# Kernel tuning notes

Hardware: AMD Instinct MI355X
Metric: run time of the kernel (lower is better)

The kernel has to match this reference:

```python
import jax, jax.numpy as jnp
import numpy as np

V_WORD, V_ENT, V_REL = 50000, 200000, 1000
B, S, CTX, T = 64, 128, 256, 10
E, D, H, C = 300, 100, 256, 3  # input_dim, triples_embedding_dim, hidden, classes
IN = E + 2 * D  # LSTM input size in graph_attention mode


def setup_inputs() -> dict:
    key = jax.random.key(0)
    ks = jax.random.split(key, 16)
    inputs = jax.random.randint(ks[0], (B, S), 0, V_WORD)
    context = jax.random.randint(ks[1], (B, CTX), 0, V_WORD)
    triples = jax.random.randint(ks[2], (B, S, T, 3), 0, V_REL)
    lengths = jax.random.randint(ks[3], (B,), 1, S + 1)  # valid lengths >= 1
    # id2_ids_batch: -1 sentinel means "no triple"; mix of -1 and valid
    id2_ids_batch = jax.random.randint(ks[4], (B, S, T), 0, 2) * 2 - 1
    embedding = jax.random.normal(ks[5], (V_WORD, E), jnp.float32) * 0.02
    embeddings_entity = jax.random.normal(ks[6], (V_ENT, D), jnp.float32) * 0.02
    embeddings_relation = jax.random.normal(ks[7], (V_REL, D), jnp.float32) * 0.02
    W_ent = jax.random.normal(ks[8], (D, 2 * D), jnp.float32) * 0.05  # entity_transformed (no bias)
    W_ih = jax.random.normal(ks[9], (4 * H, IN), jnp.float32) * 0.05
    W_hh = jax.random.normal(ks[10], (4 * H, H), jnp.float32) * 0.05
    b_lstm = jnp.zeros((4 * H,), jnp.float32)
    attn_w = jax.random.normal(ks[11], (1, H), jnp.float32) * 0.05
    attn_b = jnp.zeros((1,), jnp.float32)
    out_w = jax.random.normal(ks[12], (C, H), jnp.float32) * 0.05
    out_b = jnp.zeros((C,), jnp.float32)
    return dict(inputs=inputs, context=context, triples=triples, lengths=lengths,
                id2_ids_batch=id2_ids_batch, embedding=embedding,
                embeddings_entity=embeddings_entity, embeddings_relation=embeddings_relation,
                W_ent=W_ent, W_ih=W_ih, W_hh=W_hh, b_lstm=b_lstm,
                attn_w=attn_w, attn_b=attn_b, out_w=out_w, out_b=out_b)


def _lstm(x, W_ih, W_hh, b):
    """Single-layer unidirectional LSTM, PyTorch gate order (i,f,g,o). x: [B,S,I] -> [B,S,H]."""
    Hh = W_hh.shape[1]
    xg = jnp.einsum('bsi,gi->bsg', x, W_ih) + b  # precompute input projections [B,S,4H]
    def step(carry, xg_t):
        h, c = carry
        g = xg_t + h @ W_hh.T
        i, f, gg, o = jnp.split(g, 4, axis=-1)
        c = jax.nn.sigmoid(f) * c + jax.nn.sigmoid(i) * jnp.tanh(gg)
        h = jax.nn.sigmoid(o) * jnp.tanh(c)
        return (h, c), h
    h0 = jnp.zeros((x.shape[0], Hh), x.dtype)
    _, hs = jax.lax.scan(step, (h0, h0), jnp.swapaxes(xg, 0, 1))
    return jnp.swapaxes(hs, 0, 1)


def reference(inputs, context, triples, lengths, id2_ids_batch, embedding,
              embeddings_entity, embeddings_relation, W_ent, W_ih, W_hh, b_lstm,
              attn_w, attn_b, out_w, out_b):
    x = embedding[inputs]  # [B,S,E]
    # graph_attention branch, vectorized over (batch, token, triple)
    eh = embeddings_entity[triples[..., 0]]   # [B,S,T,D]
    et = embeddings_entity[triples[..., 1]]   # [B,S,T,D]
    er = embeddings_relation[triples[..., 2]] # [B,S,T,D]
    ht = jnp.concatenate([eh, et], axis=-1)   # [B,S,T,2D]
    tr = jnp.tanh(jnp.einsum('bstk,dk->bstd', ht, W_ent))  # entity_transformed + tanh
    e = jnp.sum(tr * er, axis=-1)             # [B,S,T]
    alpha = jax.nn.softmax(e, axis=-1)        # softmax over triples
    graph = jnp.einsum('bst,bstk->bsk', alpha, ht)  # [B,S,2D]
    valid = jnp.any(id2_ids_batch != -1, axis=-1)   # [B,S]; all -1 -> zeros (cc branch)
    graph = jnp.where(valid[..., None], graph, 0.0)
    t_in = jnp.concatenate([x, graph], axis=-1)     # [B,S,E+2D]
    out = _lstm(t_in, W_ih, W_hh, b_lstm)           # [B,S,H]
    # 'att' attention pooling, masked by lengths (pack/pad equivalent)
    mask = jnp.arange(S)[None, :] < lengths[:, None]
    scores = (jnp.einsum('bsh,oh->bso', out, attn_w) + attn_b)[..., 0]  # [B,S]
    a = jax.nn.softmax(jnp.where(mask, scores, -1e9), axis=-1)
    attended = jnp.einsum('bs,bsh->bh', a, out)     # [B,H]
    logits = attended @ out_w.T + out_b             # [B,C]
    return logits
```

## Files before the change

### kernel.cpp

```cpp
#include <hip/hip_runtime.h>
#include <cstdint>
#include <cstddef>

typedef unsigned int  uint_t;
typedef unsigned short ushort_t;

constexpr int B_  = 64;
constexpr int S_  = 128;
constexpr int D_  = 100;
constexpr int E_  = 300;
constexpr int H_  = 256;
constexpr int KIN = 512;
constexpr int NG  = 1024;
constexpr int M_  = B_ * S_;

constexpr int RW = 48;
constexpr int LW = 16;

constexpr size_t OFF_WT   = 0;
constexpr size_t OFF_FLAG = 40000;
constexpr size_t OFF_WIH  = 40960;
constexpr size_t OFF_WHH  = OFF_WIH + (size_t)NG * KIN * 2;
constexpr size_t OFF_TIN  = OFF_WHH + (size_t)128 * NG * 4;
constexpr size_t OFF_XG   = OFF_TIN + (size_t)M_ * KIN * 2;
constexpr size_t OFF_HOUT = OFF_XG + (size_t)M_ * NG * 4;

__device__ __forceinline__ float b2f(ushort_t u) {
  union { uint_t u; float f; } v; v.u = ((uint_t)u) << 16; return v.f;
}
__device__ __forceinline__ float blo(uint_t u) {
  union { uint_t u; float f; } v; v.u = u << 16; return v.f;
}
__device__ __forceinline__ float bhi(uint_t u) {
  union { uint_t u; float f; } v; v.u = u & 0xffff0000u; return v.f;
}
__device__ __forceinline__ ushort_t f2b(float f) {
  union { float f; uint_t u; } v; v.f = f;
  uint_t r = (v.u + 0x7fffu + ((v.u >> 16) & 1u)) >> 16;
  return (ushort_t)r;
}
__device__ __forceinline__ ushort_t f16bits(float f) {
  _Float16 h = (_Float16)f;
  union { _Float16 h; ushort_t u; } v; v.h = h; return v.u;
}
__device__ __forceinline__ uint_t pk16(float a, float b) {
  return (uint_t)f16bits(a) | ((uint_t)f16bits(b) << 16);
}
__device__ __forceinline__ float fast_tanh(float x) {
  float e = __expf(2.f * x);
  return 1.f - 2.f / (e + 1.f);
}
__device__ __forceinline__ float sigm(float x) {
  return 1.f / (1.f + __expf(-x));
}
__device__ __forceinline__ float ldv(const void* p, size_t i, int f32) {
  return f32 ? ((const float*)p)[i] : b2f(((const ushort_t*)p)[i]);
}

#if defined(__has_builtin)
#if __has_builtin(__builtin_amdgcn_fdot2)
#define HAVE_FDOT2 1
#endif
#endif

typedef _Float16 half2v __attribute__((ext_vector_type(2)));

__device__ __forceinline__ float dot2(uint_t w, uint_t h, float acc) {
#ifdef HAVE_FDOT2
  union { uint_t u; half2v v; } a, b; a.u = w; b.u = h;
  return __builtin_amdgcn_fdot2(a.v, b.v, acc, false);
#else
  union { uint_t u; _Float16 h[2]; } a, b; a.u = w; b.u = h;
  acc += (float)a.h[0] * (float)b.h[0];
  acc += (float)a.h[1] * (float)b.h[1];
  return acc;
#endif
}

__global__ __launch_bounds__(64) void k_detect(const uint_t* __restrict__ emb_w,
                                               char* __restrict__ ws)
{
  int tid = threadIdx.x;
  int hits = 0;
  for (int i = 0; i < 8; ++i) {
    uint_t w = emb_w[i * 64 + tid];
    uint_t e = (w >> 7) & 0xffu;
    hits += (e >= 140) ? 1 : 0;
  }
  for (int off = 32; off > 0; off >>= 1) hits += __shfl_down(hits, off);
  if (tid == 0) *(int*)(ws + OFF_FLAG) = (hits >= 32) ? 1 : 0;
}

__global__ __launch_bounds__(256) void k0_prep(
    const void* __restrict__ W_ent, const void* __restrict__ W_ih,
    const void* __restrict__ W_hh, char* __restrict__ ws)
{
  const int f32 = *(const int*)(ws + OFF_FLAG);
  int id = blockIdx.x * 256 + threadIdx.x;
  uint_t*   Wt = (uint_t*)(ws + OFF_WT);
  ushort_t* Wp = (ushort_t*)(ws + OFF_WIH);
  uint_t*   WT = (uint_t*)(ws + OFF_WHH);
  if (id < 10000) {
    int kp = id / 100, d = id % 100;
    float a = ldv(W_ent, (size_t)d * 200 + 2 * kp,     f32);
    float b = ldv(W_ent, (size_t)d * 200 + 2 * kp + 1, f32);
    Wt[id] = pk16(a, b);
  } else if (id >= 20000 && id < 20000 + NG * KIN) {
    int i = id - 20000;
    int n = i >> 9, k = i & 511;
    Wp[i] = (k < 500) ? f2b(ldv(W_ih, (size_t)n * 500 + k, f32)) : (ushort_t)0;
  } else if (id >= 20000 + NG * KIN && id < 20000 + NG * KIN + 128 * NG) {
    int i = id - 20000 - NG * KIN;
    int kk = i >> 10, j = i & 1023;
    ushort_t lo = f16bits(ldv(W_hh, (size_t)j * 256 + 2 * kk,     f32));
    ushort_t hi = f16bits(ldv(W_hh, (size_t)j * 256 + 2 * kk + 1, f32));
    WT[kk * 1024 + j] = (uint_t)lo | ((uint_t)hi << 16);
  }
}

__global__ __launch_bounds__(512) void k1_graph(
    const int* __restrict__ inputs, const int* __restrict__ triples,
    const int* __restrict__ id2, const void* __restrict__ emb,
    const void* __restrict__ ent, const void* __restrict__ rel,
    char* __restrict__ ws)
{
  __shared__ __align__(16) uint_t Wl2[10000];
  __shared__ uint_t htp[4][10][100];
  __shared__ float er_l[4][10][100];
  __shared__ float e_l[4][10];
  __shared__ float alpha_l[4][10];
  __shared__ int   trip_l[4][30];
  __shared__ int   vflag[4];

  const int tid = threadIdx.x;
  const int j   = tid >> 7;
  const int lt  = tid & 127;
  const int m   = blockIdx.x * 4 + j;
  const int f32 = *(const int*)(ws + OFF_FLAG);
  ushort_t* tin = (ushort_t*)(ws + OFF_TIN);

  if (lt < 30) trip_l[j][lt] = triples[(size_t)m * 30 + lt];
  if (lt == 0) vflag[j] = 0;
  if (lt < 10) e_l[j][lt] = 0.f;
  __syncthreads();
  if (lt < 10 && id2[(size_t)m * 10 + lt] != -1) atomicOr(&vflag[j], 1);

  {
    const uint4* src = (const uint4*)(ws + OFF_WT);
    uint4* dst = (uint4*)Wl2;
    for (int i = tid; i < 2500; i += 512) dst[i] = src[i];
  }
  for (int i = lt; i < 1000; i += 128) {
    int t = i / 100, kp = i % 100;
    int row = trip_l[j][t * 3 + (kp < 50 ? 0 : 1)];
    int off = (kp < 50) ? 2 * kp : 2 * (kp - 50);
    float x0, x1;
    if (f32) {
      float2 v = *(const float2*)((const float*)ent + (size_t)row * 100 + off);
      x0 = v.x; x1 = v.y;
    } else {
      uint_t u = *(const uint_t*)((const ushort_t*)ent + (size_t)row * 100 + off);
      x0 = blo(u); x1 = bhi(u);
    }
    htp[j][t][kp] = pk16(x0, x1);
  }
  for (int i = lt; i < 1000; i += 128) {
    int t = i / 100, d = i % 100;
    er_l[j][t][d] = ldv(rel, (size_t)trip_l[j][t * 3 + 2] * 100 + d, f32);
  }
  {
    int w = inputs[m];
    for (int c = lt; c < 300; c += 128)
      tin[(size_t)m * KIN + c] = f2b(ldv(emb, (size_t)w * E_ + c, f32));
    if (lt < 12) tin[(size_t)m * KIN + 500 + lt] = 0;
  }
  __syncthreads();

  if (lt < 125) {
    int t2 = lt / 25, d4 = lt % 25;
    int t0 = 2 * t2, t1 = t0 + 1;
    const uint_t* h0p = htp[j][t0];
    const uint_t* h1p = htp[j][t1];
    float a00 = 0, a01 = 0, a02 = 0, a03 = 0;
    float a10 = 0, a11 = 0, a12 = 0, a13 = 0;
    for (int kp = 0; kp < 100; ++kp) {
      uint4 wv = *(const uint4*)&Wl2[kp * 100 + 4 * d4];
      uint_t hp0 = h0p[kp], hp1 = h1p[kp];
      a00 = dot2(wv.x, hp0, a00); a01 = dot2(wv.y, hp0, a01);
      a02 = dot2(wv.z, hp0, a02); a03 = dot2(wv.w, hp0, a03);
      a10 = dot2(wv.x, hp1, a10); a11 = dot2(wv.y, hp1, a11);
      a12 = dot2(wv.z, hp1, a12); a13 = dot2(wv.w, hp1, a13);
    }
    int d = 4 * d4;
    float s0 = fast_tanh(a00) * er_l[j][t0][d]     + fast_tanh(a01) * er_l[j][t0][d + 1]
             + fast_tanh(a02) * er_l[j][t0][d + 2] + fast_tanh(a03) * er_l[j][t0][d + 3];
    float s1 = fast_tanh(a10) * er_l[j][t1][d]     + fast_tanh(a11) * er_l[j][t1][d + 1]
             + fast_tanh(a12) * er_l[j][t1][d + 2] + fast_tanh(a13) * er_l[j][t1][d + 3];
    atomicAdd(&e_l[j][t0], s0);
    atomicAdd(&e_l[j][t1], s1);
  }
  __syncthreads();
  if (lt == 0) {
    float mx = e_l[j][0];
    for (int t = 1; t < 10; ++t) mx = fmaxf(mx, e_l[j][t]);
    float s = 0.f;
    for (int t = 0; t < 10; ++t) { float v = __expf(e_l[j][t] - mx); alpha_l[j][t] = v; s += v; }
    float inv = 1.f / s;
    for (int t = 0; t < 10; ++t) alpha_l[j][t] *= inv;
  }
  __syncthreads();
  for (int kp = lt; kp < 100; kp += 128) {
    float g0 = 0.f, g1 = 0.f;
#pragma unroll
    for (int t = 0; t < 10; ++t) {
      union { uint_t u; _Float16 h[2]; } v; v.u = htp[j][t][kp];
      g0 += alpha_l[j][t] * (float)v.h[0];
      g1 += alpha_l[j][t] * (float)v.h[1];
    }
    if (!vflag[j]) { g0 = 0.f; g1 = 0.f; }
    tin[(size_t)m * KIN + 300 + 2 * kp]     = f2b(g0);
    tin[(size_t)m * KIN + 300 + 2 * kp + 1] = f2b(g1);
  }
}

typedef __attribute__((ext_vector_type(8))) short short8;
typedef __attribute__((ext_vector_type(4))) float f32x4;

__global__ __launch_bounds__(256) void k2_xg(
    const void* __restrict__ bl, char* __restrict__ ws)
{
  __shared__ __align__(16) ushort_t As[128 * 32];
  __shared__ __align__(16) ushort_t Bs[128 * 32];
  const ushort_t* A  = (const ushort_t*)(ws + OFF_TIN);
  const ushort_t* Bw = (const ushort_t*)(ws + OFF_WIH);
  float* xg = (float*)(ws + OFF_XG);
  const int f32 = *(const int*)(ws + OFF_FLAG);

  const int tid = threadIdx.x;
  const int m0 = blockIdx.x * 128;
  const int n0 = blockIdx.y * 128;
  const int lane = tid & 63, wv = tid >> 6;
  const int wm = wv & 1, wn = wv >> 1;
  const int g = lane >> 4, r = lane & 15;

  f32x4 acc[4][4] = {};

  for (int ks = 0; ks < 16; ++ks) {
    const int k0 = ks * 32;
    {
      int c0 = tid, c1 = tid + 256;
      uint4 a0 = *(const uint4*)(A  + (size_t)(m0 + (c0 >> 2)) * KIN + k0 + ((c0 & 3) << 3));
      uint4 a1 = *(const uint4*)(A  + (size_t)(m0 + (c1 >> 2)) * KIN + k0 + ((c1 & 3) << 3));
      uint4 b0 = *(const uint4*)(Bw + (size_t)(n0 + (c0 >> 2)) * KIN + k0 + ((c0 & 3) << 3));
      uint4 b1 = *(const uint4*)(Bw + (size_t)(n0 + (c1 >> 2)) * KIN + k0 + ((c1 & 3) << 3));
      ((uint4*)As)[c0] = a0; ((uint4*)As)[c1] = a1;
      ((uint4*)Bs)[c0] = b0; ((uint4*)Bs)[c1] = b1;
    }
    __syncthreads();
    short8 av[4], bv[4];
#pragma unroll
    for (int i = 0; i < 4; ++i)
      av[i] = *(const short8*)&As[(wm * 64 + i * 16 + r) * 32 + g * 8];
#pragma unroll
    for (int j = 0; j < 4; ++j)
      bv[j] = *(const short8*)&Bs[(wn * 64 + j * 16 + r) * 32 + g * 8];
#pragma unroll
    for (int i = 0; i < 4; ++i)
#pragma unroll
      for (int j = 0; j < 4; ++j)
        acc[i][j] = __builtin_amdgcn_mfma_f32_16x16x32_bf16(av[i], bv[j], acc[i][j], 0, 0, 0);
    __syncthreads();
  }
#pragma unroll
  for (int j = 0; j < 4; ++j) {
    int n = n0 + wn * 64 + j * 16 + r;
    float bias = ldv(bl, n, f32);
#pragma unroll
    for (int i = 0; i < 4; ++i) {
      int mrow = m0 + wm * 64 + i * 16 + g * 4;
#pragma unroll
      for (int rr = 0; rr < 4; ++rr)
        xg[(size_t)(mrow + rr) * NG + n] = acc[i][j][rr] + bias;
    }
  }
}

__global__ __attribute__((amdgpu_waves_per_eu(2, 2))) __launch_bounds__(512)
void k3_lstm(char* __restrict__ ws)
{
  extern __shared__ __align__(16) char smem[];
  uint4*    ldsw = (uint4*)smem;
  ushort_t* hbuf = (ushort_t*)(smem + 16 * 512 * 16);

  const int tid  = threadIdx.x;
  const int b    = blockIdx.x;
  const int u    = tid >> 1;
  const int half = tid & 1;
  const int kbase = half * 64;

  const uint_t* WT = (const uint_t*)(ws + OFF_WHH);
  const float* xg = (const float*)(ws + OFF_XG);
  float* hout = (float*)(ws + OFF_HOUT);

  const int row0 = u, row1 = u + 256, row2 = u + 512, row3 = u + 768;

  uint_t w0[RW], w1[RW], w2[RW], w3[RW];
#pragma unroll
  for (int q = 0; q < RW; ++q) {
    w0[q] = WT[(size_t)(kbase + q) * 1024 + row0];
    w1[q] = WT[(size_t)(kbase + q) * 1024 + row1];
    w2[q] = WT[(size_t)(kbase + q) * 1024 + row2];
    w3[q] = WT[(size_t)(kbase + q) * 1024 + row3];
  }
  {
    const int rows[4] = { row0, row1, row2, row3 };
#pragma unroll
    for (int i = 0; i < 4; ++i)
#pragma unroll
      for (int p = 0; p < 4; ++p) {
        uint4 v;
        v.x = WT[(size_t)(kbase + RW + 4 * p + 0) * 1024 + rows[i]];
        v.y = WT[(size_t)(kbase + RW + 4 * p + 1) * 1024 + rows[i]];
        v.z = WT[(size_t)(kbase + RW + 4 * p + 2) * 1024 + rows[i]];
        v.w = WT[(size_t)(kbase + RW + 4 * p + 3) * 1024 + rows[i]];
        ldsw[(i * 4 + p) * 512 + tid] = v;
      }
  }
  hbuf[tid] = 0;
  float c = 0.f;
  __syncthreads();

  const int bm = b * S_;
  const float* xp0 = xg + (size_t)bm * NG;
  float xn0 = xp0[row0], xn1 = xp0[row1], xn2 = xp0[row2], xn3 = xp0[row3];

  for (int t = 0; t < S_; ++t) {
    const int cur = t & 1;
    float x0 = xn0, x1 = xn1, x2 = xn2, x3 = xn3;
    if (t + 1 < S_) {
      const float* xq = xg + (size_t)(bm + t + 1) * NG;
      xn0 = xq[row0]; xn1 = xq[row1]; xn2 = xq[row2]; xn3 = xq[row3];
    }
    const uint_t* hb = (const uint_t*)(hbuf + cur * 256);
    float a0 = 0.f, a1 = 0.f, a2 = 0.f, a3 = 0.f;
#pragma unroll
    for (int qq = 0; qq < RW / 4; ++qq) {
      uint4 hv = *(const uint4*)&hb[kbase + 4 * qq];
      a0 = dot2(w0[4 * qq], hv.x, a0); a0 = dot2(w0[4 * qq + 1], hv.y, a0);
      a0 = dot2(w0[4 * qq + 2], hv.z, a0); a0 = dot2(w0[4 * qq + 3], hv.w, a0);
      a1 = dot2(w1[4 * qq], hv.x, a1); a1 = dot2(w1[4 * qq + 1], hv.y, a1);
      a1 = dot2(w1[4 * qq + 2], hv.z, a1); a1 = dot2(w1[4 * qq + 3], hv.w, a1);
      a2 = dot2(w2[4 * qq], hv.x, a2); a2 = dot2(w2[4 * qq + 1], hv.y, a2);
      a2 = dot2(w2[4 * qq + 2], hv.z, a2); a2 = dot2(w2[4 * qq + 3], hv.w, a2);
      a3 = dot2(w3[4 * qq], hv.x, a3); a3 = dot2(w3[4 * qq + 1], hv.y, a3);
      a3 = dot2(w3[4 * qq + 2], hv.z, a3); a3 = dot2(w3[4 * qq + 3], hv.w, a3);
    }
#pragma unroll
    for (int p = 0; p < 4; ++p) {
      uint4 hv = *(const uint4*)&hb[kbase + RW + 4 * p];
      uint4 v0 = ldsw[(0 * 4 + p) * 512 + tid];
      uint4 v1 = ldsw[(1 * 4 + p) * 512 + tid];
      uint4 v2 = ldsw[(2 * 4 + p) * 512 + tid];
      uint4 v3 = ldsw[(3 * 4 + p) * 512 + tid];
      a0 = dot2(v0.x, hv.x, a0); a0 = dot2(v0.y, hv.y, a0);
      a0 = dot2(v0.z, hv.z, a0); a0 = dot2(v0.w, hv.w, a0);
      a1 = dot2(v1.x, hv.x, a1); a1 = dot2(v1.y, hv.y, a1);
      a1 = dot2(v1.z, hv.z, a1); a1 = dot2(v1.w, hv.w, a1);
      a2 = dot2(v2.x, hv.x, a2); a2 = dot2(v2.y, hv.y, a2);
      a2 = dot2(v2.z, hv.z, a2); a2 = dot2(v2.w, hv.w, a2);
      a3 = dot2(v3.x, hv.x, a3); a3 = dot2(v3.y, hv.y, a3);
      a3 = dot2(v3.z, hv.z, a3); a3 = dot2(v3.w, hv.w, a3);
    }
    float gi = a0 + __shfl_xor(a0, 1) + x0;
    float gf = a1 + __shfl_xor(a1, 1) + x1;
    float gg = a2 + __shfl_xor(a2, 1) + x2;
    float go = a3 + __shfl_xor(a3, 1) + x3;
    c = sigm(gf) * c + sigm(gi) * fast_tanh(gg);
    float hv = sigm(go) * fast_tanh(c);
    if (!half) {
      hout[(size_t)(bm + t) * H_ + u] = hv;
      hbuf[(cur ^ 1) * 256 + u] = f16bits(hv);
    }
    __syncthreads();
  }
}

__global__ __launch_bounds__(256) void k4_attn(
    const int* __restrict__ lengths, const void* __restrict__ attn_w,
    const void* __restrict__ attn_b, const void* __restrict__ out_w,
    const void* __restrict__ out_b, const char* __restrict__ ws,
    void* __restrict__ out)
{
  __shared__ float aw[256];
  __shared__ float sc[128];
  __shared__ float at[256];
  __shared__ float red[256];

  const int tid = threadIdx.x;
  const int b = blockIdx.x;
  const int f32 = *(const int*)(ws + OFF_FLAG);
  const float* hout = (const float*)(ws + OFF_HOUT);
  const int bm = b * S_;

  aw[tid] = ldv(attn_w, tid, f32);
  __syncthreads();
  if (tid < 128) {
    const float* hp = hout + (size_t)(bm + tid) * H_;
    float acc = 0.f;
    for (int k = 0; k < 256; k += 4) {
      float4 h4 = *(const float4*)(hp + k);
      acc += h4.x * aw[k] + h4.y * aw[k + 1] + h4.z * aw[k + 2] + h4.w * aw[k + 3];
    }
    sc[tid] = acc + ldv(attn_b, 0, f32);
  }
  __syncthreads();
  if (tid == 0) {
    int len = lengths[b];
    float mx = -3.4e38f;
    for (int s = 0; s < len; ++s) mx = fmaxf(mx, sc[s]);
    float sum = 0.f;
    for (int s = 0; s < 128; ++s) {
      float v = (s < len) ? __expf(sc[s] - mx) : 0.f;
      sc[s] = v; sum += v;
    }
    float inv = 1.f / sum;
    for (int s = 0; s < 128; ++s) sc[s] *= inv;
  }
  __syncthreads();
  {
    float acc = 0.f;
    for (int s = 0; s < 128; ++s)
      acc += sc[s] * hout[(size_t)(bm + s) * H_ + tid];
    at[tid] = acc;
  }
  __syncthreads();
  for (int cc = 0; cc < 3; ++cc) {
    red[tid] = at[tid] * ldv(out_w, cc * 256 + tid, f32);
    __syncthreads();
    for (int off = 128; off > 0; off >>= 1) {
      if (tid < off) red[tid] += red[tid + off];
      __syncthreads();
    }
    if (tid == 0) {
      float v = red[0] + ldv(out_b, cc, f32);
      if (f32) ((float*)out)[b * 3 + cc] = v;
      else     ((ushort_t*)out)[b * 3 + cc] = f2b(v);
    }
    __syncthreads();
  }
}

extern "C" void kernel_launch(void* const* d_in, const int* in_sizes, int n_in,
                              void* d_out, int out_size, void* d_ws, size_t ws_size,
                              hipStream_t stream)
{
  const int* inputs  = (const int*)d_in[0];
  const int* triples = (const int*)d_in[2];
  const int* lengths = (const int*)d_in[3];
  const int* id2     = (const int*)d_in[4];
  const void* emb    = d_in[5];
  const void* ent    = d_in[6];
  const void* rel    = d_in[7];
  const void* W_ent  = d_in[8];
  const void* W_ih   = d_in[9];
  const void* W_hh   = d_in[10];
  const void* b_lstm = d_in[11];
  const void* attn_w = d_in[12];
  const void* attn_b = d_in[13];
  const void* out_w  = d_in[14];
  const void* out_b  = d_in[15];
  char* ws = (char*)d_ws;

  constexpr int K3_SMEM = 16 * 512 * 16 + 2 * 256 * 2;
  static bool attr_set = false;
  if (!attr_set) {
    (void)hipFuncSetAttribute((const void*)k3_lstm,
                              hipFuncAttributeMaxDynamicSharedMemorySize, K3_SMEM);
    attr_set = true;
  }

  k_detect<<<dim3(1), dim3(64), 0, stream>>>((const uint_t*)emb, ws);
  k0_prep<<<dim3(2639), dim3(256), 0, stream>>>(W_ent, W_ih, W_hh, ws);
  k1_graph<<<dim3(M_ / 4), dim3(512), 0, stream>>>(inputs, triples, id2, emb, ent, rel, ws);
  k2_xg<<<dim3(64, 8), dim3(256), 0, stream>>>(b_lstm, ws);
  k3_lstm<<<dim3(B_), dim3(512), K3_SMEM, stream>>>(ws);
  k4_attn<<<dim3(B_), dim3(256), 0, stream>>>(lengths, attn_w, attn_b, out_w, out_b, ws, d_out);
}
```

Before: 526.0 us.

## Process two batch rows per LSTM block to reuse register-resident weights

The recurrent LSTM kernel now handles two sequences per workgroup, launching half as many blocks. Each weight value held in registers or LDS is applied to two hidden-state vectors, so every weight load feeds twice the dot-product work. This trades parallelism (only 32 blocks on a many-CU GPU) for more per-step arithmetic. Per-step latency may rise, since each thread does twice the dot2 work serially, and the extra accumulators add register pressure.

```diff
diff --git a/kernel.cpp b/kernel.cpp
--- a/kernel.cpp
+++ b/kernel.cpp
@@ -293,7 +293,8 @@
   ushort_t* hbuf = (ushort_t*)(smem + 16 * 512 * 16);
 
   const int tid  = threadIdx.x;
-  const int b    = blockIdx.x;
+  const int b0   = blockIdx.x * 2;
+  const int b1   = b0 + 1;
   const int u    = tid >> 1;
   const int half = tid & 1;
   const int kbase = half * 64;
@@ -327,59 +328,93 @@
       }
   }
   hbuf[tid] = 0;
-  float c = 0.f;
-  __syncthreads();
-
-  const int bm = b * S_;
-  const float* xp0 = xg + (size_t)bm * NG;
-  float xn0 = xp0[row0], xn1 = xp0[row1], xn2 = xp0[row2], xn3 = xp0[row3];
+  hbuf[512 + tid] = 0;
+  float c0 = 0.f, c1 = 0.f;
+  __syncthreads();
+
+  const int bm0 = b0 * S_, bm1 = b1 * S_;
+  const float* xpa = xg + (size_t)bm0 * NG;
+  const float* xpb = xg + (size_t)bm1 * NG;
+  float xa0 = xpa[row0], xa1 = xpa[row1], xa2 = xpa[row2], xa3 = xpa[row3];
+  float xb0 = xpb[row0], xb1 = xpb[row1], xb2 = xpb[row2], xb3 = xpb[row3];
 
   for (int t = 0; t < S_; ++t) {
     const int cur = t & 1;
-    float x0 = xn0, x1 = xn1, x2 = xn2, x3 = xn3;
+    float x00 = xa0, x01 = xa1, x02 = xa2, x03 = xa3;
+    float x10 = xb0, x11 = xb1, x12 = xb2, x13 = xb3;
     if (t + 1 < S_) {
-      const float* xq = xg + (size_t)(bm + t + 1) * NG;
-      xn0 = xq[row0]; xn1 = xq[row1]; xn2 = xq[row2]; xn3 = xq[row3];
-    }
-    const uint_t* hb = (const uint_t*)(hbuf + cur * 256);
-    float a0 = 0.f, a1 = 0.f, a2 = 0.f, a3 = 0.f;
+      const float* xqa = xg + (size_t)(bm0 + t + 1) * NG;
+      const float* xqb = xg + (size_t)(bm1 + t + 1) * NG;
+      xa0 = xqa[row0]; xa1 = xqa[row1]; xa2 = xqa[row2]; xa3 = xqa[row3];
+      xb0 = xqb[row0]; xb1 = xqb[row1]; xb2 = xqb[row2]; xb3 = xqb[row3];
+    }
+    const uint_t* hbA = (const uint_t*)(hbuf + cur * 256);
+    const uint_t* hbB = (const uint_t*)(hbuf + 512 + cur * 256);
+    float a00 = 0.f, a01 = 0.f, a02 = 0.f, a03 = 0.f;
+    float a10 = 0.f, a11 = 0.f, a12 = 0.f, a13 = 0.f;
 #pragma unroll
     for (int qq = 0; qq < RW / 4; ++qq) {
-      uint4 hv = *(const uint4*)&hb[kbase + 4 * qq];
-      a0 = dot2(w0[4 * qq], hv.x, a0); a0 = dot2(w0[4 * qq + 1], hv.y, a0);
-      a0 = dot2(w0[4 * qq + 2], hv.z, a0); a0 = dot2(w0[4 * qq + 3], hv.w, a0);
-      a1 = dot2(w1[4 * qq], hv.x, a1); a1 = dot2(w1[4 * qq + 1], hv.y, a1);
-      a1 = dot2(w1[4 * qq + 2], hv.z, a1); a1 = dot2(w1[4 * qq + 3], hv.w, a1);
-      a2 = dot2(w2[4 * qq], hv.x, a2); a2 = dot2(w2[4 * qq + 1], hv.y, a2);
-      a2 = dot2(w2[4 * qq + 2], hv.z, a2); a2 = dot2(w2[4 * qq + 3], hv.w, a2);
-      a3 = dot2(w3[4 * qq], hv.x, a3); a3 = dot2(w3[4 * qq + 1], hv.y, a3);
-      a3 = dot2(w3[4 * qq + 2], hv.z, a3); a3 = dot2(w3[4 * qq + 3], hv.w, a3);
+      uint4 ha = *(const uint4*)&hbA[kbase + 4 * qq];
+      uint4 hc = *(const uint4*)&hbB[kbase + 4 * qq];
+      a00 = dot2(w0[4 * qq], ha.x, a00); a00 = dot2(w0[4 * qq + 1], ha.y, a00);
+      a00 = dot2(w0[4 * qq + 2], ha.z, a00); a00 = dot2(w0[4 * qq + 3], ha.w, a00);
+      a10 = dot2(w0[4 * qq], hc.x, a10); a10 = dot2(w0[4 * qq + 1], hc.y, a10);
+      a10 = dot2(w0[4 * qq + 2], hc.z, a10); a10 = dot2(w0[4 * qq + 3], hc.w, a10);
+      a01 = dot2(w1[4 * qq], ha.x, a01); a01 = dot2(w1[4 * qq + 1], ha.y, a01);
+      a01 = dot2(w1[4 * qq + 2], ha.z, a01); a01 = dot2(w1[4 * qq + 3], ha.w, a01);
+      a11 = dot2(w1[4 * qq], hc.x, a11); a11 = dot2(w1[4 * qq + 1], hc.y, a11);
+      a11 = dot2(w1[4 * qq + 2], hc.z, a11); a11 = dot2(w1[4 * qq + 3], hc.w, a11);
+      a02 = dot2(w2[4 * qq], ha.x, a02); a02 = dot2(w2[4 * qq + 1], ha.y, a02);
+      a02 = dot2(w2[4 * qq + 2], ha.z, a02); a02 = dot2(w2[4 * qq + 3], ha.w, a02);
+      a12 = dot2(w2[4 * qq], hc.x, a12); a12 = dot2(w2[4 * qq + 1], hc.y, a12);
+      a12 = dot2(w2[4 * qq + 2], hc.z, a12); a12 = dot2(w2[4 * qq + 3], hc.w, a12);
+      a03 = dot2(w3[4 * qq], ha.x, a03); a03 = dot2(w3[4 * qq + 1], ha.y, a03);
+      a03 = dot2(w3[4 * qq + 2], ha.z, a03); a03 = dot2(w3[4 * qq + 3], ha.w, a03);
+      a13 = dot2(w3[4 * qq], hc.x, a13); a13 = dot2(w3[4 * qq + 1], hc.y, a13);
+      a13 = dot2(w3[4 * qq + 2], hc.z, a13); a13 = dot2(w3[4 * qq + 3], hc.w, a13);
     }
 #pragma unroll
     for (int p = 0; p < 4; ++p) {
-      uint4 hv = *(const uint4*)&hb[kbase + RW + 4 * p];
+      uint4 ha = *(const uint4*)&hbA[kbase + RW + 4 * p];
+      uint4 hc = *(const uint4*)&hbB[kbase + RW + 4 * p];
       uint4 v0 = ldsw[(0 * 4 + p) * 512 + tid];
       uint4 v1 = ldsw[(1 * 4 + p) * 512 + tid];
       uint4 v2 = ldsw[(2 * 4 + p) * 512 + tid];
       uint4 v3 = ldsw[(3 * 4 + p) * 512 + tid];
-      a0 = dot2(v0.x, hv.x, a0); a0 = dot2(v0.y, hv.y, a0);
-      a0 = dot2(v0.z, hv.z, a0); a0 = dot2(v0.w, hv.w, a0);
-      a1 = dot2(v1.x, hv.x, a1); a1 = dot2(v1.y, hv.y, a1);
-      a1 = dot2(v1.z, hv.z, a1); a1 = dot2(v1.w, hv.w, a1);
-      a2 = dot2(v2.x, hv.x, a2); a2 = dot2(v2.y, hv.y, a2);
-      a2 = dot2(v2.z, hv.z, a2); a2 = dot2(v2.w, hv.w, a2);
-      a3 = dot2(v3.x, hv.x, a3); a3 = dot2(v3.y, hv.y, a3);
-      a3 = dot2(v3.z, hv.z, a3); a3 = dot2(v3.w, hv.w, a3);
-    }
-    float gi = a0 + __shfl_xor(a0, 1) + x0;
-    float gf = a1 + __shfl_xor(a1, 1) + x1;
-    float gg = a2 + __shfl_xor(a2, 1) + x2;
-    float go = a3 + __shfl_xor(a3, 1) + x3;
-    c = sigm(gf) * c + sigm(gi) * fast_tanh(gg);
-    float hv = sigm(go) * fast_tanh(c);
+      a00 = dot2(v0.x, ha.x, a00); a00 = dot2(v0.y, ha.y, a00);
+      a00 = dot2(v0.z, ha.z, a00); a00 = dot2(v0.w, ha.w, a00);
+      a10 = dot2(v0.x, hc.x, a10); a10 = dot2(v0.y, hc.y, a10);
+      a10 = dot2(v0.z, hc.z, a10); a10 = dot2(v0.w, hc.w, a10);
+      a01 = dot2(v1.x, ha.x, a01); a01 = dot2(v1.y, ha.y, a01);
+      a01 = dot2(v1.z, ha.z, a01); a01 = dot2(v1.w, ha.w, a01);
+      a11 = dot2(v1.x, hc.x, a11); a11 = dot2(v1.y, hc.y, a11);
+      a11 = dot2(v1.z, hc.z, a11); a11 = dot2(v1.w, hc.w, a11);
+      a02 = dot2(v2.x, ha.x, a02); a02 = dot2(v2.y, ha.y, a02);
+      a02 = dot2(v2.z, ha.z, a02); a02 = dot2(v2.w, ha.w, a02);
+      a12 = dot2(v2.x, hc.x, a12); a12 = dot2(v2.y, hc.y, a12);
+      a12 = dot2(v2.z, hc.z, a12); a12 = dot2(v2.w, hc.w, a12);
+      a03 = dot2(v3.x, ha.x, a03); a03 = dot2(v3.y, ha.y, a03);
+      a03 = dot2(v3.z, ha.z, a03); a03 = dot2(v3.w, ha.w, a03);
+      a13 = dot2(v3.x, hc.x, a13); a13 = dot2(v3.y, hc.y, a13);
+      a13 = dot2(v3.z, hc.z, a13); a13 = dot2(v3.w, hc.w, a13);
+    }
+    float gi0 = a00 + __shfl_xor(a00, 1) + x00;
+    float gf0 = a01 + __shfl_xor(a01, 1) + x01;
+    float gg0 = a02 + __shfl_xor(a02, 1) + x02;
+    float go0 = a03 + __shfl_xor(a03, 1) + x03;
+    float gi1 = a10 + __shfl_xor(a10, 1) + x10;
+    float gf1 = a11 + __shfl_xor(a11, 1) + x11;
+    float gg1 = a12 + __shfl_xor(a12, 1) + x12;
+    float go1 = a13 + __shfl_xor(a13, 1) + x13;
+    c0 = sigm(gf0) * c0 + sigm(gi0) * fast_tanh(gg0);
+    c1 = sigm(gf1) * c1 + sigm(gi1) * fast_tanh(gg1);
+    float hv0 = sigm(go0) * fast_tanh(c0);
+    float hv1 = sigm(go1) * fast_tanh(c1);
     if (!half) {
-      hout[(size_t)(bm + t) * H_ + u] = hv;
-      hbuf[(cur ^ 1) * 256 + u] = f16bits(hv);
+      hout[(size_t)(bm0 + t) * H_ + u] = hv0;
+      hout[(size_t)(bm1 + t) * H_ + u] = hv1;
+      hbuf[(cur ^ 1) * 256 + u] = f16bits(hv0);
+      hbuf[512 + (cur ^ 1) * 256 + u] = f16bits(hv1);
     }
     __syncthreads();
   }
@@ -471,7 +506,7 @@
   const void* out_b  = d_in[15];
   char* ws = (char*)d_ws;
 
-  constexpr int K3_SMEM = 16 * 512 * 16 + 2 * 256 * 2;
+  constexpr int K3_SMEM = 16 * 512 * 16 + 4 * 256 * 2;
   static bool attr_set = false;
   if (!attr_set) {
     (void)hipFuncSetAttribute((const void*)k3_lstm,
@@ -483,6 +518,6 @@
   k0_prep<<<dim3(2639), dim3(256), 0, stream>>>(W_ent, W_ih, W_hh, ws);
   k1_graph<<<dim3(M_ / 4), dim3(512), 0, stream>>>(inputs, triples, id2, emb, ent, rel, ws);
   k2_xg<<<dim3(64, 8), dim3(256), 0, stream>>>(b_lstm, ws);
-  k3_lstm<<<dim3(B_), dim3(512), K3_SMEM, stream>>>(ws);
+  k3_lstm<<<dim3(B_ / 2), dim3(512), K3_SMEM, stream>>>(ws);
   k4_attn<<<dim3(B_), dim3(256), 0, stream>>>(lengths, attn_w, attn_b, out_w, out_b, ws, d_out);
 }
```

After: 760.9 us. 1.45x slower.
